# Optimization experiments

Measured on AMD Instinct MI355X. Metric: run time of the kernel, lower is better.

The kernel has to match this reference:

```python
import jax, jax.numpy as jnp
import numpy as np

B, T, F = 256, 192, 8
CARD0, CARD1 = 1000, 100
E0, E1 = 32, 16
H = 512
D_IN = F + E0 + E1  # 56


def _glorot(key, shape):
    fan_in, fan_out = shape[0], shape[-1]
    lim = jnp.sqrt(6.0 / (fan_in + fan_out))
    return jax.random.uniform(key, shape, jnp.float32, -lim, lim)


def setup_inputs() -> dict:
    key = jax.random.key(0)
    ks = jax.random.split(key, 16)
    return {
        "x_cont": jax.random.normal(ks[0], (B, T, F), jnp.float32),
        "cat0": jax.random.randint(ks[1], (B, T), 0, CARD0),
        "cat1": jax.random.randint(ks[2], (B, T), 0, CARD1),
        "emb0": _glorot(ks[3], (CARD0, E0)),
        "emb1": _glorot(ks[4], (CARD1, E1)),
        "Wk1": _glorot(ks[5], (D_IN, 4 * H)),
        "Wr1": _glorot(ks[6], (H, 4 * H)),
        "b1": jnp.zeros((4 * H,), jnp.float32).at[H:2 * H].set(1.0),  # unit_forget_bias
        "Wk2": _glorot(ks[7], (H, 4 * H)),
        "Wr2": _glorot(ks[8], (H, 4 * H)),
        "b2": jnp.zeros((4 * H,), jnp.float32).at[H:2 * H].set(1.0),
        "Wmu": _glorot(ks[9], (H, 1)),
        "bmu": _glorot(ks[10], (1, 1))[0],
        "Wsig": _glorot(ks[11], (H, 1)),
        "bsig": _glorot(ks[12], (1, 1))[0],
    }


def _lstm(x, Wk, Wr, b):
    # x: [B, T, D]; Keras gate order i, f, g(c), o; zero initial states (inference mode,
    # dropout/recurrent_dropout inactive when training=False).
    xz = jnp.einsum('btd,dk->btk', x, Wk) + b  # precompute input projection for all steps
    h0 = jnp.zeros((x.shape[0], H), x.dtype)

    def step(carry, z_t):
        h, c = carry
        z = z_t + h @ Wr  # [B, 4H]
        i, f, g, o = jnp.split(z, 4, axis=-1)
        i = jax.nn.sigmoid(i)
        f = jax.nn.sigmoid(f)
        g = jnp.tanh(g)
        o = jax.nn.sigmoid(o)
        c = f * c + i * g
        h = o * jnp.tanh(c)
        return (h, c), h

    _, hs = jax.lax.scan(step, (h0, h0), jnp.swapaxes(xz, 0, 1))  # [T, B, H]
    return jnp.swapaxes(hs, 0, 1)


def reference(x_cont, cat0, cat1, emb0, emb1, Wk1, Wr1, b1, Wk2, Wr2, b2, Wmu, bmu, Wsig, bsig):
    x = jnp.concatenate([x_cont, emb0[cat0], emb1[cat1]], axis=-1)  # [B, T, 56]
    x = _lstm(x, Wk1, Wr1, b1)
    x = _lstm(x, Wk2, Wr2, b2)
    mu = x @ Wmu + bmu                      # count_data=False -> raw mu
    sigma = jax.nn.softplus(x @ Wsig + bsig)
    return (mu, sigma)
```

## Files before the change

### kernel.cpp

```cpp
#include <hip/hip_runtime.h>
#include <math.h>

#define Bsz 256
#define Tsz 192
#define Fc 8
#define E0c 32
#define E1c 16
#define Hc 512
#define G4 2048
#define DINP 64
#define K1t 576
#define K2t 1024
#define NBLK 256
#define LBLK 32
#define KPAD1 584
#define KPAD2 1032
#define LDSB_BYTES (64 * KPAD2 * 2)
#define FTEAM 64
#define WD_WAIT (1 << 17)

typedef __attribute__((ext_vector_type(8))) short short8;
typedef __attribute__((ext_vector_type(4))) float f32x4;

template<int N> struct IC { static constexpr int v = N; };
template<int C, int CMAX, typename F>
__device__ __forceinline__ void static_for(F&& f) {
    if constexpr (C < CMAX) {
        f(IC<C>{});
        static_for<C + 1, CMAX>(f);
    }
}

static __device__ __forceinline__ float bf2f(ushort u) {
    return __uint_as_float(((uint)u) << 16);
}
static __device__ __forceinline__ ushort f2bf(float f) {
    uint u = __float_as_uint(f);
    u = (u + 0x7fffu + ((u >> 16) & 1u)) >> 16;
    return (ushort)u;
}

static __device__ __forceinline__ uint poll_sc1(const uint* p) {
    uint v;
    asm volatile("global_load_dword %0, %1, off sc1\n\t"
                 "s_waitcnt vmcnt(0)"
                 : "=v"(v) : "v"((unsigned long long)p) : "memory");
    return v;
}
static __device__ __forceinline__ void store_slot_sc1(uint* p, uint v) {
    asm volatile("global_store_dword %0, %1, off sc1"
                 :: "v"((unsigned long long)p), "v"(v) : "memory");
}

static __device__ __forceinline__ void wait_flags(const uint* f, uint tg) {
    const uint* p = f + (threadIdx.x & 31);
    int it = 0;
    while (true) {
        uint v = poll_sc1(p);
        if (__all((int)(v >= tg))) break;
        if (++it >= WD_WAIT) break;
        __builtin_amdgcn_s_sleep(1);
    }
}

__global__ __launch_bounds__(256) void build_x_kernel(
    const float* __restrict__ x_cont, const int* __restrict__ cat0,
    const int* __restrict__ cat1, const float* __restrict__ emb0,
    const float* __restrict__ emb1, ushort* __restrict__ x_bf)
{
    int idx = blockIdx.x * 256 + threadIdx.x;
    if (idx >= Tsz * Bsz * DINP) return;
    int d = idx & 63;
    int row = idx >> 6;
    int t = row >> 8;
    int b = row & 255;
    float v = 0.f;
    if (d < Fc)                  v = x_cont[(b * Tsz + t) * Fc + d];
    else if (d < Fc + E0c)       v = emb0[cat0[b * Tsz + t] * E0c + (d - Fc)];
    else if (d < Fc + E0c + E1c) v = emb1[cat1[b * Tsz + t] * E1c + (d - Fc - E0c)];
    x_bf[idx] = f2bf(v);
}

__global__ __launch_bounds__(256) void transpose_w_kernel(
    const float* __restrict__ in, ushort* __restrict__ out, int K, int ldout, int coff)
{
    __shared__ float tile[32][33];
    int k0 = blockIdx.x * 32;
    int n0 = blockIdx.y * 32;
    int tx = threadIdx.x & 31, ty = threadIdx.x >> 5;
    #pragma unroll
    for (int p = 0; p < 4; ++p) {
        int k = k0 + ty + p * 8;
        tile[ty + p * 8][tx] = (k < K) ? in[k * G4 + n0 + tx] : 0.f;
    }
    __syncthreads();
    #pragma unroll
    for (int p = 0; p < 4; ++p) {
        int nl = ty + p * 8;
        out[(size_t)(n0 + nl) * ldout + coff + k0 + tx] = f2bf(tile[tx][nl]);
    }
}

template<int KS_IN, int KS_TOT, int LDA_IN, int KPADv, bool HAS_DEP>
static __device__ __forceinline__ void run_layer(
    const ushort* __restrict__ Ain,
    ushort* __restrict__ hbuf,
    const ushort* __restrict__ hz,
    const ushort* __restrict__ Wt,
    const float* __restrict__ bias,
    ushort* B_lds,
    const uint* dep_flags,
    const uint* own_flags, uint* my_flag,
    int m0, int j0)
{
    constexpr int KS_R = KS_TOT - KS_IN;
    constexpr int KL = KS_TOT * 32;
    constexpr int SEGS = KL / 8;
    int tid = threadIdx.x;
    int lane = tid & 63, wv = tid >> 6;
    int lane15 = lane & 15, quad = lane >> 4;

    for (int i = tid; i < 64 * SEGS; i += 256) {
        int row = i / SEGS, seg = i - row * SEGS;
        int gz = (row >> 4) * Hc + j0 + (row & 15);
        *(uint4*)&B_lds[row * KPADv + seg * 8] =
            *(const uint4*)(Wt + (size_t)gz * KL + seg * 8);
    }
    __syncthreads();

    float bgate[4];
    #pragma unroll
    for (int gt = 0; gt < 4; ++gt) bgate[gt] = bias[gt * Hc + j0 + lane15];
    float cst[4] = {0.f, 0.f, 0.f, 0.f};

    int arow = m0 + wv * 16 + lane15;
    int crow0 = m0 + wv * 16 + quad * 4;

    for (int t = 0; t < Tsz; ++t) {
        f32x4 acc[4];
        #pragma unroll
        for (int gt = 0; gt < 4; ++gt) acc[gt] = (f32x4){0.f, 0.f, 0.f, 0.f};

        if constexpr (HAS_DEP) {
            if (tid < 64) wait_flags(dep_flags, (uint)(t + 1));
            __syncthreads();
        }
        {
            const ushort* p0 = Ain + ((size_t)t * Bsz + arow) * LDA_IN + quad * 8;
            uint4 bufA[KS_IN];
            static_for<0, KS_IN>([&](auto Kc) {
                constexpr int ks = decltype(Kc)::v;
                bufA[ks] = *(const uint4*)(p0 + ks * 32);
            });
            asm volatile("" ::: "memory");
            static_for<0, KS_IN>([&](auto Kc) {
                constexpr int ks = decltype(Kc)::v;
                short8 av = __builtin_bit_cast(short8, bufA[ks]);
                #pragma unroll
                for (int gt = 0; gt < 4; ++gt) {
                    short8 bfr = *(const short8*)&B_lds[(gt * 16 + lane15) * KPADv + ks * 32 + quad * 8];
                    acc[gt] = __builtin_amdgcn_mfma_f32_16x16x32_bf16(av, bfr, acc[gt], 0, 0, 0);
                }
            });
        }

        if (t) {
            if (tid < 64) wait_flags(own_flags, (uint)t);
            __syncthreads();
        }
        {
            const ushort* p1base = (t > 0) ? (hbuf + (size_t)(t - 1) * Bsz * Hc) : hz;
            const ushort* p1 = p1base + (size_t)arow * Hc + quad * 8;
            uint4 bufB[KS_R];
            static_for<0, KS_R>([&](auto Kc) {
                constexpr int ks = decltype(Kc)::v;
                bufB[ks] = *(const uint4*)(p1 + ks * 32);
            });
            asm volatile("" ::: "memory");
            static_for<0, KS_R>([&](auto Kc) {
                constexpr int ks = decltype(Kc)::v;
                short8 av = __builtin_bit_cast(short8, bufB[ks]);
                #pragma unroll
                for (int gt = 0; gt < 4; ++gt) {
                    short8 bfr = *(const short8*)&B_lds[(gt * 16 + lane15) * KPADv + (KS_IN + ks) * 32 + quad * 8];
                    acc[gt] = __builtin_amdgcn_mfma_f32_16x16x32_bf16(av, bfr, acc[gt], 0, 0, 0);
                }
            });
        }

        uint hv[4];
        #pragma unroll
        for (int r = 0; r < 4; ++r) {
            float zi = acc[0][r] + bgate[0];
            float zf = acc[1][r] + bgate[1];
            float zg = acc[2][r] + bgate[2];
            float zo = acc[3][r] + bgate[3];
            float ig = 1.f / (1.f + __expf(-zi));
            float fg = 1.f / (1.f + __expf(-zf));
            float gg = tanhf(zg);
            float og = 1.f / (1.f + __expf(-zo));
            float cn = fg * cst[r] + ig * gg;
            cst[r] = cn;
            float hn = og * tanhf(cn);
            hv[r] = (uint)f2bf(hn);
        }
        {
            unsigned long long hb = (unsigned long long)
                &hbuf[((size_t)t * Bsz + crow0) * Hc + j0 + lane15];
            asm volatile(
                "global_store_short %0, %1, off sc1\n\t"
                "global_store_short %0, %2, off offset:1024 sc1\n\t"
                "global_store_short %0, %3, off offset:2048 sc1\n\t"
                "global_store_short %0, %4, off offset:3072 sc1\n\t"
                "s_waitcnt vmcnt(0)"
                :: "v"(hb), "v"(hv[0]), "v"(hv[1]), "v"(hv[2]), "v"(hv[3])
                : "memory");
        }

        __syncthreads();
        if (tid == 0)
            store_slot_sc1(my_flag, (uint)(t + 1));
    }
}

__global__ __launch_bounds__(256, 1) void deepar_persistent(
    const ushort* __restrict__ x_bf,
    const ushort* __restrict__ Wt1, const ushort* __restrict__ Wt2,
    const float* __restrict__ b1, const float* __restrict__ b2,
    ushort* __restrict__ h1, ushort* __restrict__ h2,
    const ushort* __restrict__ hz,
    const float* __restrict__ Wmu, const float* __restrict__ bmu,
    const float* __restrict__ Wsig, const float* __restrict__ bsig,
    float* __restrict__ out, uint* __restrict__ flags)
{
    extern __shared__ ushort B_lds[];

    int bid = blockIdx.x;
    int xcd = bid & 7;
    int g = xcd >> 1;
    int role = xcd & 1;
    int jb = bid >> 3;
    int m0 = g * 64;
    int j0 = jb * 16;

    uint* f1 = flags + (g * 2 + 0) * FTEAM;
    uint* f2 = flags + (g * 2 + 1) * FTEAM;

    if (role == 0) {
        run_layer<2, 18, DINP, KPAD1, false>(x_bf, h1, hz, Wt1, b1, B_lds,
                                             nullptr, f1, f1 + jb, m0, j0);
        return;
    }
    run_layer<16, 32, Hc, KPAD2, true>(h1, h2, hz, Wt2, b2, B_lds,
                                       f1, f2, f2 + jb, m0, j0);

    if (threadIdx.x < 64) wait_flags(f2, (uint)Tsz);
    __syncthreads();

    int lane = threadIdx.x & 63, wv = threadIdx.x >> 6;
    float wm[8], wsg[8];
    #pragma unroll
    for (int i = 0; i < 8; ++i) {
        wm[i] = Wmu[lane * 8 + i];
        wsg[i] = Wsig[lane * 8 + i];
    }
    float bmu0 = bmu[0], bsg0 = bsig[0];
    for (int i = jb * 4 + wv; i < 64 * Tsz; i += 128) {
        int b = m0 + (i & 63);
        int t = i >> 6;
        const ushort* hp = h2 + ((size_t)t * Bsz + b) * Hc + lane * 8;
        short8 hvv = *(const short8*)hp;
        float smu = 0.f, ssg = 0.f;
        #pragma unroll
        for (int e = 0; e < 8; ++e) {
            float f = bf2f((ushort)hvv[e]);
            smu += f * wm[e];
            ssg += f * wsg[e];
        }
        #pragma unroll
        for (int off = 32; off > 0; off >>= 1) {
            smu += __shfl_down(smu, off, 64);
            ssg += __shfl_down(ssg, off, 64);
        }
        if (lane == 0) {
            int oi = b * Tsz + t;
            float sg = ssg + bsg0;
            float sp = sg > 0.f ? sg + log1pf(__expf(-sg)) : log1pf(__expf(sg));
            out[oi] = smu + bmu0;
            out[Bsz * Tsz + oi] = sp;
        }
    }
}

extern "C" void kernel_launch(void* const* d_in, const int* in_sizes, int n_in,
                              void* d_out, int out_size, void* d_ws, size_t ws_size,
                              hipStream_t stream) {
    const float* x_cont = (const float*)d_in[0];
    const int*   cat0   = (const int*)d_in[1];
    const int*   cat1   = (const int*)d_in[2];
    const float* emb0   = (const float*)d_in[3];
    const float* emb1   = (const float*)d_in[4];
    const float* Wk1    = (const float*)d_in[5];
    const float* Wr1    = (const float*)d_in[6];
    const float* b1     = (const float*)d_in[7];
    const float* Wk2    = (const float*)d_in[8];
    const float* Wr2    = (const float*)d_in[9];
    const float* b2     = (const float*)d_in[10];
    const float* Wmu    = (const float*)d_in[11];
    const float* bmu    = (const float*)d_in[12];
    const float* Wsig   = (const float*)d_in[13];
    const float* bsig   = (const float*)d_in[14];
    float* out = (float*)d_out;

    const size_t flags_bytes = 8 * FTEAM * 4;

    char* ws = (char*)d_ws;
    uint*   flags = (uint*)ws;                                 ws += flags_bytes;
    ushort* x_bf  = (ushort*)ws;                               ws += (size_t)Tsz * Bsz * DINP * 2;
    ushort* Wt1   = (ushort*)ws;                               ws += (size_t)G4 * K1t * 2;
    ushort* Wt2   = (ushort*)ws;                               ws += (size_t)G4 * K2t * 2;
    ushort* h1    = (ushort*)ws;                               ws += (size_t)Tsz * Bsz * Hc * 2;
    ushort* h2    = (ushort*)ws;                               ws += (size_t)Tsz * Bsz * Hc * 2;
    ushort* hz    = (ushort*)ws;                               ws += (size_t)Bsz * Hc * 2;

    hipMemsetAsync(flags, 0, flags_bytes, stream);
    hipMemsetAsync(hz, 0, (size_t)Bsz * Hc * 2, stream);

    build_x_kernel<<<(Tsz * Bsz * DINP + 255) / 256, 256, 0, stream>>>(
        x_cont, cat0, cat1, emb0, emb1, x_bf);
    transpose_w_kernel<<<dim3(2, 64), 256, 0, stream>>>(Wk1, Wt1, 56, K1t, 0);
    transpose_w_kernel<<<dim3(16, 64), 256, 0, stream>>>(Wr1, Wt1, Hc, K1t, DINP);
    transpose_w_kernel<<<dim3(16, 64), 256, 0, stream>>>(Wk2, Wt2, Hc, K2t, 0);
    transpose_w_kernel<<<dim3(16, 64), 256, 0, stream>>>(Wr2, Wt2, Hc, K2t, Hc);

    hipFuncSetAttribute((const void*)deepar_persistent,
                        hipFuncAttributeMaxDynamicSharedMemorySize, LDSB_BYTES);
    deepar_persistent<<<dim3(NBLK), dim3(256), LDSB_BYTES, stream>>>(
        x_bf, Wt1, Wt2, b1, b2, h1, h2, hz, Wmu, bmu, Wsig, bsig, out, flags);
}
```

Before: 1.374 ms.

## Replace per-step flag barriers with sentinel-based data polling on hidden states

Removes the per-timestep flag counters, block-wide barriers and store waits that coordinated producer and consumer blocks. Instead, the h1/h2 buffers are pre-filled with 0xFFFF sentinels, and consumers repeatedly load their operand tiles with sc1 loads until no bf16 element equals the sentinel. This cuts the store-wait, flag store, poll and syncthreads round trip from the recurrent critical path. In exchange it adds two full memsets of the large hidden-state buffers. It also relies on 0xFFFF (a NaN bit pattern) never being a legitimate output, and on the stores becoming visible in a consistent way.

```diff
diff --git a/kernel.cpp b/kernel.cpp
--- a/kernel.cpp
+++ b/kernel.cpp
@@ -12,15 +12,14 @@
 #define K1t 576
 #define K2t 1024
 #define NBLK 256
-#define LBLK 32
 #define KPAD1 584
 #define KPAD2 1032
 #define LDSB_BYTES (64 * KPAD2 * 2)
-#define FTEAM 64
 #define WD_WAIT (1 << 17)
 
 typedef __attribute__((ext_vector_type(8))) short short8;
 typedef __attribute__((ext_vector_type(4))) float f32x4;
+typedef __attribute__((ext_vector_type(4))) uint u32x4;
 
 template<int N> struct IC { static constexpr int v = N; };
 template<int C, int CMAX, typename F>
@@ -40,24 +39,34 @@
     return (ushort)u;
 }
 
-static __device__ __forceinline__ uint poll_sc1(const uint* p) {
-    uint v;
-    asm volatile("global_load_dword %0, %1, off sc1\n\t"
-                 "s_waitcnt vmcnt(0)"
-                 : "=v"(v) : "v"((unsigned long long)p) : "memory");
-    return v;
-}
-static __device__ __forceinline__ void store_slot_sc1(uint* p, uint v) {
-    asm volatile("global_store_dword %0, %1, off sc1"
-                 :: "v"((unsigned long long)p), "v"(v) : "memory");
-}
-
-static __device__ __forceinline__ void wait_flags(const uint* f, uint tg) {
-    const uint* p = f + (threadIdx.x & 31);
+static __device__ __forceinline__ u32x4 ld128_sc1(const void* p) {
+    u32x4 r;
+    asm volatile("global_load_dwordx4 %0, %1, off sc1"
+                 : "=v"(r) : "v"((unsigned long long)p));
+    return r;
+}
+static __device__ __forceinline__ uint sent2(uint u) {
+    return (uint)(((u & 0xFFFFu) == 0xFFFFu) | ((u >> 16) == 0xFFFFu));
+}
+
+template<int KS>
+static __device__ __forceinline__ void load_gated(const ushort* p, u32x4* buf) {
     int it = 0;
     while (true) {
-        uint v = poll_sc1(p);
-        if (__all((int)(v >= tg))) break;
+        static_for<0, KS>([&](auto Kc) {
+            constexpr int ks = decltype(Kc)::v;
+            buf[ks] = ld128_sc1(p + ks * 32);
+        });
+        asm volatile("s_waitcnt vmcnt(0)" ::: "memory");
+        __builtin_amdgcn_sched_barrier(0);
+        uint bad = 0;
+        static_for<0, KS>([&](auto Kc) {
+            constexpr int ks = decltype(Kc)::v;
+            u32x4 b = buf[ks];
+            #pragma unroll
+            for (int d = 0; d < 4; ++d) bad |= sent2(b[d]);
+        });
+        if (!__any((int)bad)) break;
         if (++it >= WD_WAIT) break;
         __builtin_amdgcn_s_sleep(1);
     }
@@ -101,7 +110,7 @@
     }
 }
 
-template<int KS_IN, int KS_TOT, int LDA_IN, int KPADv, bool HAS_DEP>
+template<int KS_IN, int KS_TOT, int LDA_IN, int KPADv, bool A_GATED>
 static __device__ __forceinline__ void run_layer(
     const ushort* __restrict__ Ain,
     ushort* __restrict__ hbuf,
@@ -109,8 +118,6 @@
     const ushort* __restrict__ Wt,
     const float* __restrict__ bias,
     ushort* B_lds,
-    const uint* dep_flags,
-    const uint* own_flags, uint* my_flag,
     int m0, int j0)
 {
     constexpr int KS_R = KS_TOT - KS_IN;
@@ -141,18 +148,18 @@
         #pragma unroll
         for (int gt = 0; gt < 4; ++gt) acc[gt] = (f32x4){0.f, 0.f, 0.f, 0.f};
 
-        if constexpr (HAS_DEP) {
-            if (tid < 64) wait_flags(dep_flags, (uint)(t + 1));
-            __syncthreads();
-        }
         {
             const ushort* p0 = Ain + ((size_t)t * Bsz + arow) * LDA_IN + quad * 8;
-            uint4 bufA[KS_IN];
-            static_for<0, KS_IN>([&](auto Kc) {
-                constexpr int ks = decltype(Kc)::v;
-                bufA[ks] = *(const uint4*)(p0 + ks * 32);
-            });
-            asm volatile("" ::: "memory");
+            u32x4 bufA[KS_IN];
+            if constexpr (A_GATED) {
+                load_gated<KS_IN>(p0, bufA);
+            } else {
+                static_for<0, KS_IN>([&](auto Kc) {
+                    constexpr int ks = decltype(Kc)::v;
+                    bufA[ks] = __builtin_bit_cast(u32x4, *(const uint4*)(p0 + ks * 32));
+                });
+                asm volatile("" ::: "memory");
+            }
             static_for<0, KS_IN>([&](auto Kc) {
                 constexpr int ks = decltype(Kc)::v;
                 short8 av = __builtin_bit_cast(short8, bufA[ks]);
@@ -164,19 +171,19 @@
             });
         }
 
-        if (t) {
-            if (tid < 64) wait_flags(own_flags, (uint)t);
-            __syncthreads();
-        }
         {
-            const ushort* p1base = (t > 0) ? (hbuf + (size_t)(t - 1) * Bsz * Hc) : hz;
-            const ushort* p1 = p1base + (size_t)arow * Hc + quad * 8;
-            uint4 bufB[KS_R];
-            static_for<0, KS_R>([&](auto Kc) {
-                constexpr int ks = decltype(Kc)::v;
-                bufB[ks] = *(const uint4*)(p1 + ks * 32);
-            });
-            asm volatile("" ::: "memory");
+            u32x4 bufB[KS_R];
+            if (t == 0) {
+                const ushort* p1 = hz + (size_t)arow * Hc + quad * 8;
+                static_for<0, KS_R>([&](auto Kc) {
+                    constexpr int ks = decltype(Kc)::v;
+                    bufB[ks] = __builtin_bit_cast(u32x4, *(const uint4*)(p1 + ks * 32));
+                });
+                asm volatile("" ::: "memory");
+            } else {
+                const ushort* p1 = hbuf + ((size_t)(t - 1) * Bsz + arow) * Hc + quad * 8;
+                load_gated<KS_R>(p1, bufB);
+            }
             static_for<0, KS_R>([&](auto Kc) {
                 constexpr int ks = decltype(Kc)::v;
                 short8 av = __builtin_bit_cast(short8, bufB[ks]);
@@ -211,15 +218,10 @@
                 "global_store_short %0, %1, off sc1\n\t"
                 "global_store_short %0, %2, off offset:1024 sc1\n\t"
                 "global_store_short %0, %3, off offset:2048 sc1\n\t"
-                "global_store_short %0, %4, off offset:3072 sc1\n\t"
-                "s_waitcnt vmcnt(0)"
+                "global_store_short %0, %4, off offset:3072 sc1"
                 :: "v"(hb), "v"(hv[0]), "v"(hv[1]), "v"(hv[2]), "v"(hv[3])
                 : "memory");
         }
-
-        __syncthreads();
-        if (tid == 0)
-            store_slot_sc1(my_flag, (uint)(t + 1));
     }
 }
 
@@ -231,7 +233,7 @@
     const ushort* __restrict__ hz,
     const float* __restrict__ Wmu, const float* __restrict__ bmu,
     const float* __restrict__ Wsig, const float* __restrict__ bsig,
-    float* __restrict__ out, uint* __restrict__ flags)
+    float* __restrict__ out)
 {
     extern __shared__ ushort B_lds[];
 
@@ -243,19 +245,11 @@
     int m0 = g * 64;
     int j0 = jb * 16;
 
-    uint* f1 = flags + (g * 2 + 0) * FTEAM;
-    uint* f2 = flags + (g * 2 + 1) * FTEAM;
-
     if (role == 0) {
-        run_layer<2, 18, DINP, KPAD1, false>(x_bf, h1, hz, Wt1, b1, B_lds,
-                                             nullptr, f1, f1 + jb, m0, j0);
+        run_layer<2, 18, DINP, KPAD1, false>(x_bf, h1, hz, Wt1, b1, B_lds, m0, j0);
         return;
     }
-    run_layer<16, 32, Hc, KPAD2, true>(h1, h2, hz, Wt2, b2, B_lds,
-                                       f1, f2, f2 + jb, m0, j0);
-
-    if (threadIdx.x < 64) wait_flags(f2, (uint)Tsz);
-    __syncthreads();
+    run_layer<16, 32, Hc, KPAD2, true>(h1, h2, hz, Wt2, b2, B_lds, m0, j0);
 
     int lane = threadIdx.x & 63, wv = threadIdx.x >> 6;
     float wm[8], wsg[8];
@@ -269,7 +263,22 @@
         int b = m0 + (i & 63);
         int t = i >> 6;
         const ushort* hp = h2 + ((size_t)t * Bsz + b) * Hc + lane * 8;
-        short8 hvv = *(const short8*)hp;
+        u32x4 rv;
+        {
+            int it = 0;
+            while (true) {
+                rv = ld128_sc1(hp);
+                asm volatile("s_waitcnt vmcnt(0)" ::: "memory");
+                __builtin_amdgcn_sched_barrier(0);
+                uint bad = 0;
+                #pragma unroll
+                for (int d = 0; d < 4; ++d) bad |= sent2(rv[d]);
+                if (!__any((int)bad)) break;
+                if (++it >= WD_WAIT) break;
+                __builtin_amdgcn_s_sleep(1);
+            }
+        }
+        short8 hvv = __builtin_bit_cast(short8, rv);
         float smu = 0.f, ssg = 0.f;
         #pragma unroll
         for (int e = 0; e < 8; ++e) {
@@ -312,18 +321,18 @@
     const float* bsig   = (const float*)d_in[14];
     float* out = (float*)d_out;
 
-    const size_t flags_bytes = 8 * FTEAM * 4;
+    const size_t h_bytes = (size_t)Tsz * Bsz * Hc * 2;
 
     char* ws = (char*)d_ws;
-    uint*   flags = (uint*)ws;                                 ws += flags_bytes;
     ushort* x_bf  = (ushort*)ws;                               ws += (size_t)Tsz * Bsz * DINP * 2;
     ushort* Wt1   = (ushort*)ws;                               ws += (size_t)G4 * K1t * 2;
     ushort* Wt2   = (ushort*)ws;                               ws += (size_t)G4 * K2t * 2;
-    ushort* h1    = (ushort*)ws;                               ws += (size_t)Tsz * Bsz * Hc * 2;
-    ushort* h2    = (ushort*)ws;                               ws += (size_t)Tsz * Bsz * Hc * 2;
+    ushort* h1    = (ushort*)ws;                               ws += h_bytes;
+    ushort* h2    = (ushort*)ws;                               ws += h_bytes;
     ushort* hz    = (ushort*)ws;                               ws += (size_t)Bsz * Hc * 2;
 
-    hipMemsetAsync(flags, 0, flags_bytes, stream);
+    hipMemsetAsync(h1, 0xFF, h_bytes, stream);
+    hipMemsetAsync(h2, 0xFF, h_bytes, stream);
     hipMemsetAsync(hz, 0, (size_t)Bsz * Hc * 2, stream);
 
     build_x_kernel<<<(Tsz * Bsz * DINP + 255) / 256, 256, 0, stream>>>(
@@ -336,5 +345,5 @@
     hipFuncSetAttribute((const void*)deepar_persistent,
                         hipFuncAttributeMaxDynamicSharedMemorySize, LDSB_BYTES);
     deepar_persistent<<<dim3(NBLK), dim3(256), LDSB_BYTES, stream>>>(
-        x_bf, Wt1, Wt2, b1, b2, h1, h2, hz, Wmu, bmu, Wsig, bsig, out, flags);
-}
+        x_bf, Wt1, Wt2, b1, b2, h1, h2, hz, Wmu, bmu, Wsig, bsig, out);
+}
```

Result: slower. 1.896 ms (+38.0%).
